# Optimization experiments

Measured on AMD Instinct MI355X. Metric: run time of the kernel, lower is better.

## Reference

```python
import jax, jax.numpy as jnp
import numpy as np

LN_EPS = 1e-5

def setup_inputs() -> dict:
    key = jax.random.key(0)
    ks = jax.random.split(key, 10)
    N, E, H, V, L, OUT, G = 100000, 600000, 128, 65, 4, 32, 64
    x_tokens = jax.random.randint(ks[0], (N, 2), 0, V, dtype=jnp.int32)
    edge_index = jax.random.randint(ks[1], (2, E), 0, N, dtype=jnp.int32)
    batch = jnp.sort(jax.random.randint(ks[2], (N,), 0, G)).astype(jnp.int64)
    s = 0.05
    key_emb = jax.random.normal(ks[3], (V, H), jnp.float32) * s
    val_emb = jax.random.normal(ks[4], (V, H), jnp.float32) * s
    Ws = jax.random.normal(ks[5], (L, H, H), jnp.float32) * (1.0 / np.sqrt(H))
    bs = jax.random.normal(ks[6], (L, H), jnp.float32) * s
    ln_g = jnp.ones((L, H), jnp.float32)
    ln_b = jnp.zeros((L, H), jnp.float32)
    out_W = jax.random.normal(ks[7], (OUT, H), jnp.float32) * (1.0 / np.sqrt(H))
    return {"x_tokens": x_tokens, "edge_index": edge_index, "batch": batch,
            "key_emb": key_emb, "val_emb": val_emb, "Ws": Ws, "bs": bs,
            "ln_g": ln_g, "ln_b": ln_b, "out_W": out_W}

def _layer_norm(x, g, b):
    mu = jnp.mean(x, axis=-1, keepdims=True)
    var = jnp.mean(jnp.square(x - mu), axis=-1, keepdims=True)
    return (x - mu) * jax.lax.rsqrt(var + LN_EPS) * g + b

def reference(x_tokens, edge_index, batch, key_emb, val_emb, Ws, bs, ln_g, ln_b, out_W):
    N = x_tokens.shape[0]
    L = Ws.shape[0]
    # layer-0: key + value embedding lookup -> [N, H]
    x = key_emb[x_tokens[:, 0]] + val_emb[x_tokens[:, 1]]
    # GCN normalization with self-loops (computed once; edges fixed per layer)
    loop = jnp.arange(N, dtype=edge_index.dtype)
    src = jnp.concatenate([edge_index[0], loop])  # [E+N]
    dst = jnp.concatenate([edge_index[1], loop])
    deg = jax.ops.segment_sum(jnp.ones_like(dst, dtype=x.dtype), dst, num_segments=N)
    dis = jnp.where(deg > 0, jax.lax.rsqrt(jnp.maximum(deg, 1.0)), 0.0)
    norm = (dis[src] * dis[dst])[:, None]  # [E+N, 1]
    for i in range(L):
        xw = x @ Ws[i]  # [N, H]
        agg = jax.ops.segment_sum(norm * xw[src], dst, num_segments=N) + bs[i]
        new_x = jax.nn.relu(agg)          # use_activation
        x = x + new_x                      # use_residual
        x = _layer_norm(x, ln_g[i], ln_b[i])  # use_layer_norm
    logits = x @ out_W.T  # Linear(bias=False) -> [N, out_dim]
    return logits
```

## Files before the change

### kernel.cpp

```cpp
#include <hip/hip_runtime.h>

#define H 128
#define LN_EPS 1e-5f

typedef unsigned short u16;
typedef unsigned int u32;
typedef __attribute__((ext_vector_type(8))) short bf16x8;
typedef __attribute__((ext_vector_type(4))) float f32x4;

__device__ __forceinline__ float bflo(u32 u){ return __uint_as_float(u << 16); }
__device__ __forceinline__ float bfhi(u32 u){ return __uint_as_float(u & 0xFFFF0000u); }
__device__ __forceinline__ float bf1(u16 u){ return __uint_as_float(((u32)u) << 16); }
__device__ __forceinline__ u16 f2bu(float f){
  u32 u = __float_as_uint(f);
  return (u16)((u + 0x7FFFu + ((u >> 16) & 1u)) >> 16);
}

__device__ __forceinline__ float ldf(const void* p, int i, bool isbf){
  return isbf ? bf1(reinterpret_cast<const u16*>(p)[i])
              : reinterpret_cast<const float*>(p)[i];
}


__global__ void k_convert(const void* __restrict__ kemb, const void* __restrict__ vemb,
                          const void* __restrict__ Ws,   const void* __restrict__ bs,
                          const void* __restrict__ lng,  const void* __restrict__ lnb,
                          const void* __restrict__ outW,
                          float* __restrict__ kemb_f, float* __restrict__ vemb_f,
                          u16* __restrict__ W_c, float* __restrict__ bs_f,
                          float* __restrict__ lng_f, float* __restrict__ lnb_f,
                          u16* __restrict__ outW_b, int* __restrict__ flag,
                          int V, int L, int OUT){
  bool isbf = (*reinterpret_cast<const u32*>(lng) == 0x3F803F80u);
  if (blockIdx.x == 0 && threadIdx.x == 0) flag[0] = isbf ? 1 : 0;
  int i = blockIdx.x * blockDim.x + threadIdx.x;
  int nEmb = V * H;
  int nW   = L * H * H;
  int nVec = L * H;
  int nOut = OUT * H;
  if (i < nEmb){ kemb_f[i] = ldf(kemb, i, isbf); vemb_f[i] = ldf(vemb, i, isbf); }
  if (i < nW){
    int j = i & 7, lane = (i >> 3) & 63, g = i >> 9;
    int s = g & 3, cg = (g >> 2) & 7, l = g >> 5;
    int k = s * 32 + (lane >> 4) * 8 + j;
    int n = cg * 16 + (lane & 15);
    W_c[i] = f2bu(ldf(Ws, l * H * H + k * H + n, isbf));
  }
  if (i < nVec){ bs_f[i] = ldf(bs, i, isbf); lng_f[i] = ldf(lng, i, isbf);
                 lnb_f[i] = ldf(lnb, i, isbf); }
  if (i < nOut){ outW_b[i] = f2bu(ldf(outW, i, isbf)); }
}


__global__ void k_count(const int* __restrict__ dst, int E, int* __restrict__ deg){
  int i = blockIdx.x * blockDim.x + threadIdx.x;
  if (i < E) atomicAdd(&deg[dst[i]], 1);
}

__device__ __forceinline__ int paddedLen(int d){ return (d + 4) & ~3; }

__global__ void k_bsum(const int* __restrict__ deg, int* __restrict__ bsum, int N){
  __shared__ int sh[256];
  int i = blockIdx.x * 256 + threadIdx.x;
  sh[threadIdx.x] = (i < N) ? paddedLen(deg[i]) : 0;
  __syncthreads();
  for (int off = 128; off > 0; off >>= 1){
    if (threadIdx.x < off) sh[threadIdx.x] += sh[threadIdx.x + off];
    __syncthreads();
  }
  if (threadIdx.x == 0) bsum[blockIdx.x] = sh[0];
}

__global__ void k_bscan(int* __restrict__ bsum, int nb){
  __shared__ int sh[1024];
  int t = threadIdx.x;
  sh[t] = (t < nb) ? bsum[t] : 0;
  __syncthreads();
  for (int off = 1; off < 1024; off <<= 1){
    int add = (t >= off) ? sh[t - off] : 0;
    __syncthreads();
    sh[t] += add;
    __syncthreads();
  }
  if (t < nb) bsum[t] = (t > 0) ? sh[t - 1] : 0;
}

__global__ void k_scan2(const int* __restrict__ deg, const int* __restrict__ bsum,
                        int* __restrict__ row_ptr, float* __restrict__ dis,
                        int* __restrict__ cursor, int2* __restrict__ csr, int N){
  __shared__ int sh[256];
  int i = blockIdx.x * 256 + threadIdx.x;
  int d = (i < N) ? deg[i] : 0;
  int v = (i < N) ? paddedLen(d) : 0;
  sh[threadIdx.x] = v;
  __syncthreads();
  for (int off = 1; off < 256; off <<= 1){
    int add = (threadIdx.x >= off) ? sh[threadIdx.x - off] : 0;
    __syncthreads();
    sh[threadIdx.x] += add;
    __syncthreads();
  }
  int excl = sh[threadIdx.x] - v + bsum[blockIdx.x];
  if (i < N){
    row_ptr[i] = excl;
    float r = rsqrtf((float)(d + 1));
    dis[i] = r;
    cursor[i] = 1;
    csr[excl] = make_int2(i * (H / 2), __float_as_int(r * r));
    for (int p = excl + d + 1; p < excl + v; p++)
      csr[p] = make_int2(0, 0);
  }
  if (i == N - 1) row_ptr[N] = excl + v;
}

__global__ void k_fill(const int* __restrict__ src, const int* __restrict__ dst, int E,
                       const float* __restrict__ dis, const int* __restrict__ row_ptr,
                       int* __restrict__ cursor, int2* __restrict__ csr){
  int i = blockIdx.x * blockDim.x + threadIdx.x;
  if (i >= E) return;
  int s = src[i], d = dst[i];
  int pos = atomicAdd(&cursor[d], 1);
  csr[row_ptr[d] + pos] = make_int2(s * (H / 2), __float_as_int(dis[s] * dis[d]));
}


__global__ __launch_bounds__(256) void k_embed(const int* __restrict__ tok,
                        const float* __restrict__ kemb, const float* __restrict__ vemb,
                        u16* __restrict__ xb, int N){
  int n = blockIdx.x * 4 + (threadIdx.x >> 6);
  if (n >= N) return;
  int h0 = (threadIdx.x & 63) * 2;
  int t0 = tok[n * 2], t1 = tok[n * 2 + 1];
  float2 k2 = *reinterpret_cast<const float2*>(&kemb[t0 * H + h0]);
  float2 v2 = *reinterpret_cast<const float2*>(&vemb[t1 * H + h0]);
  *reinterpret_cast<u32*>(&xb[(size_t)n * H + h0]) =
      (u32)f2bu(k2.x + v2.x) | ((u32)f2bu(k2.y + v2.y) << 16);
}


__global__ __launch_bounds__(256) void k_gemm(const u16* __restrict__ xb,
                                              const u16* __restrict__ Wc,
                                              u16* __restrict__ xw, int npairs){
  int wid = threadIdx.x >> 6, lane = threadIdx.x & 63;
  int sp = wid >> 1;
  int ch = wid & 1;
  int r = lane & 15, kq = lane >> 4;
  bf16x8 wf[4][4];
  #pragma unroll
  for (int c = 0; c < 4; c++)
    #pragma unroll
    for (int s = 0; s < 4; s++)
      wf[c][s] = *reinterpret_cast<const bf16x8*>(
          Wc + (size_t)((((ch * 4 + c) * 4 + s) * 64 + lane) << 3));
  for (int p = blockIdx.x; p < npairs; p += gridDim.x){
    int node0 = (p * 2 + sp) << 4;
    const u16* xrow = xb + (size_t)node0 * H + r * H + kq * 8;
    bf16x8 xf[4];
    #pragma unroll
    for (int s = 0; s < 4; s++)
      xf[s] = *reinterpret_cast<const bf16x8*>(xrow + s * 32);
    f32x4 acc[4] = {{0,0,0,0},{0,0,0,0},{0,0,0,0},{0,0,0,0}};
    #pragma unroll
    for (int s = 0; s < 4; s++)
      #pragma unroll
      for (int c = 0; c < 4; c++)
        acc[c] = __builtin_amdgcn_mfma_f32_16x16x32_bf16(wf[c][s], xf[s], acc[c], 0, 0, 0);
    u16* orow = xw + (size_t)(node0 + r) * H + ch * 64 + kq * 4;
    #pragma unroll
    for (int c = 0; c < 4; c++){
      u32 lo = (u32)f2bu(acc[c][0]) | ((u32)f2bu(acc[c][1]) << 16);
      u32 hi = (u32)f2bu(acc[c][2]) | ((u32)f2bu(acc[c][3]) << 16);
      *reinterpret_cast<uint2*>(orow + c * 16) = make_uint2(lo, hi);
    }
  }
}


__global__ __launch_bounds__(256) void k_gather(const u32* __restrict__ xw32,
    const int* __restrict__ row_ptr, const int2* __restrict__ csr,
    const float* __restrict__ bias, const float* __restrict__ gamma,
    const float* __restrict__ beta,
    u16* __restrict__ xb, int N){
  int lane = threadIdx.x & 63;
  int w = blockIdx.x * 4 + (threadIdx.x >> 6);
  int n0 = w * 2;
  if (n0 >= N) return;
  bool two = (n0 + 1 < N);
  int h0 = lane * 2;
  const int4* csr4 = reinterpret_cast<const int4*>(csr);
  int rs0 = __builtin_amdgcn_readfirstlane(row_ptr[n0]);
  int rm  = __builtin_amdgcn_readfirstlane(row_ptr[n0 + 1]);
  int re1 = two ? __builtin_amdgcn_readfirstlane(row_ptr[n0 + 2]) : rm;
  int len0 = rm - rs0, len1 = re1 - rm;
  int common = min(len0, len1);
  u32 xv0 = *reinterpret_cast<const u32*>(&xb[(size_t)n0 * H + h0]);
  u32 xv1 = two ? *reinterpret_cast<const u32*>(&xb[(size_t)(n0 + 1) * H + h0]) : 0u;
  float2 b2 = *reinterpret_cast<const float2*>(&bias[h0]);
  float2 g2 = *reinterpret_cast<const float2*>(&gamma[h0]);
  float2 t2 = *reinterpret_cast<const float2*>(&beta[h0]);
  float a00 = 0.f, a01 = 0.f, a10 = 0.f, a11 = 0.f;
#define EDGE(CX, CY, A0, A1) { \
    u32 cx = (u32)__builtin_amdgcn_readfirstlane(CX); \
    float wgt = __uint_as_float((u32)__builtin_amdgcn_readfirstlane(CY)); \
    u32 v = xw32[cx + lane]; \
    A0 = fmaf(wgt, bflo(v), A0); A1 = fmaf(wgt, bfhi(v), A1); }
  int i = 0;
  for (; i < common; i += 4){
    int4 ca = csr4[(rs0 + i) >> 1], cb = csr4[((rs0 + i) >> 1) + 1];
    int4 da = csr4[(rm + i) >> 1],  db = csr4[((rm + i) >> 1) + 1];
    EDGE(ca.x, ca.y, a00, a01) EDGE(da.x, da.y, a10, a11)
    EDGE(ca.z, ca.w, a00, a01) EDGE(da.z, da.w, a10, a11)
    EDGE(cb.x, cb.y, a00, a01) EDGE(db.x, db.y, a10, a11)
    EDGE(cb.z, cb.w, a00, a01) EDGE(db.z, db.w, a10, a11)
  }
  for (; i < len0; i += 4){
    int4 ca = csr4[(rs0 + i) >> 1], cb = csr4[((rs0 + i) >> 1) + 1];
    EDGE(ca.x, ca.y, a00, a01) EDGE(ca.z, ca.w, a00, a01)
    EDGE(cb.x, cb.y, a00, a01) EDGE(cb.z, cb.w, a00, a01)
  }
  for (; i < len1; i += 4){
    int4 da = csr4[(rm + i) >> 1], db = csr4[((rm + i) >> 1) + 1];
    EDGE(da.x, da.y, a10, a11) EDGE(da.z, da.w, a10, a11)
    EDGE(db.x, db.y, a10, a11) EDGE(db.z, db.w, a10, a11)
  }
#undef EDGE
  float v0 = fmaxf(a00 + b2.x, 0.f), v1 = fmaxf(a01 + b2.y, 0.f);
  v0 += bflo(xv0); v1 += bfhi(xv0);
  float u0 = fmaxf(a10 + b2.x, 0.f), u1 = fmaxf(a11 + b2.y, 0.f);
  u0 += bflo(xv1); u1 += bfhi(xv1);
  float s0 = v0 + v1, s1 = u0 + u1;
  #pragma unroll
  for (int off = 32; off > 0; off >>= 1){
    s0 += __shfl_xor(s0, off);
    s1 += __shfl_xor(s1, off);
  }
  float mu0 = s0 * (1.f / 128.f), mu1 = s1 * (1.f / 128.f);
  float d00 = v0 - mu0, d01 = v1 - mu0;
  float d10 = u0 - mu1, d11 = u1 - mu1;
  float q0 = d00 * d00 + d01 * d01, q1 = d10 * d10 + d11 * d11;
  #pragma unroll
  for (int off = 32; off > 0; off >>= 1){
    q0 += __shfl_xor(q0, off);
    q1 += __shfl_xor(q1, off);
  }
  float inv0 = rsqrtf(q0 * (1.f / 128.f) + LN_EPS);
  float inv1 = rsqrtf(q1 * (1.f / 128.f) + LN_EPS);
  float o00 = d00 * inv0 * g2.x + t2.x, o01 = d01 * inv0 * g2.y + t2.y;
  *reinterpret_cast<u32*>(&xb[(size_t)n0 * H + h0]) =
      (u32)f2bu(o00) | ((u32)f2bu(o01) << 16);
  if (two){
    float o10 = d10 * inv1 * g2.x + t2.x, o11 = d11 * inv1 * g2.y + t2.y;
    *reinterpret_cast<u32*>(&xb[(size_t)(n0+1) * H + h0]) =
        (u32)f2bu(o10) | ((u32)f2bu(o11) << 16);
  }
}


__global__ __launch_bounds__(256) void k_out(const u16* __restrict__ xb,
    const u16* __restrict__ oWb, u16* __restrict__ out16, float* __restrict__ outf,
    const int* __restrict__ flag, int nstrips){
  int wid = threadIdx.x >> 6, lane = threadIdx.x & 63;
  int r = lane & 15, kq = lane >> 4;
  bool isbf = (flag[0] != 0);
  bf16x8 wf[2][4];
  #pragma unroll
  for (int ct = 0; ct < 2; ct++)
    #pragma unroll
    for (int s = 0; s < 4; s++)
      wf[ct][s] = *reinterpret_cast<const bf16x8*>(
          oWb + (ct * 16 + r) * H + s * 32 + kq * 8);
  for (int strip = blockIdx.x * 4 + wid; strip < nstrips; strip += gridDim.x * 4){
    const u16* xrow = xb + (size_t)strip * 16 * H + r * H + kq * 8;
    bf16x8 xf[4];
    #pragma unroll
    for (int s = 0; s < 4; s++)
      xf[s] = *reinterpret_cast<const bf16x8*>(xrow + s * 32);
    f32x4 acc[2] = {{0,0,0,0},{0,0,0,0}};
    #pragma unroll
    for (int s = 0; s < 4; s++)
      #pragma unroll
      for (int ct = 0; ct < 2; ct++)
        acc[ct] = __builtin_amdgcn_mfma_f32_16x16x32_bf16(wf[ct][s], xf[s], acc[ct], 0, 0, 0);
    int node = strip * 16 + r;
    if (isbf){
      #pragma unroll
      for (int ct = 0; ct < 2; ct++){
        u32 lo = (u32)f2bu(acc[ct][0]) | ((u32)f2bu(acc[ct][1]) << 16);
        u32 hi = (u32)f2bu(acc[ct][2]) | ((u32)f2bu(acc[ct][3]) << 16);
        *reinterpret_cast<uint2*>(out16 + (size_t)node * 32 + ct * 16 + kq * 4) =
            make_uint2(lo, hi);
      }
    } else {
      #pragma unroll
      for (int ct = 0; ct < 2; ct++)
        *reinterpret_cast<f32x4*>(outf + (size_t)node * 32 + ct * 16 + kq * 4) = acc[ct];
    }
  }
}


extern "C" void kernel_launch(void* const* d_in, const int* in_sizes, int n_in,
                              void* d_out, int out_size, void* d_ws, size_t ws_size,
                              hipStream_t stream){
  const int*  x_tokens = (const int*)d_in[0];
  const int*  edge_idx = (const int*)d_in[1];
  const void* kemb = d_in[3];
  const void* vemb = d_in[4];
  const void* Ws   = d_in[5];
  const void* bs   = d_in[6];
  const void* lng  = d_in[7];
  const void* lnb  = d_in[8];
  const void* outW = d_in[9];

  int N   = in_sizes[0] / 2;
  int E   = in_sizes[1] / 2;
  int V   = in_sizes[3] / H;
  int L   = in_sizes[5] / (H * H);
  int OUT = in_sizes[9] / H;

  char* ws = (char*)d_ws;
  size_t off = 0;
  auto alloc = [&](size_t bytes) -> void* {
    void* p = ws + off;
    off += (bytes + 255) & ~(size_t)255;
    return p;
  };
  u16*   xb     = (u16*)  alloc((size_t)N * H * 2);
  u16*   xw     = (u16*)  alloc((size_t)N * H * 2);
  int*   deg    = (int*)  alloc((size_t)N * 4);
  int*   cursor = (int*)  alloc((size_t)N * 4);
  int*   row_ptr= (int*)  alloc((size_t)(N + 1) * 4);
  float* dis    = (float*)alloc((size_t)N * 4);
  int*   bsum   = (int*)  alloc(1024 * 4);
  int2*  csr    = (int2*) alloc(((size_t)E + 4 * (size_t)N) * 8);
  float* kemb_f = (float*)alloc((size_t)V * H * 4);
  float* vemb_f = (float*)alloc((size_t)V * H * 4);
  u16*   W_c    = (u16*)  alloc((size_t)L * H * H * 2);
  float* bs_f   = (float*)alloc((size_t)L * H * 4);
  float* lng_f  = (float*)alloc((size_t)L * H * 4);
  float* lnb_f  = (float*)alloc((size_t)L * H * 4);
  u16*   outW_b = (u16*)  alloc((size_t)OUT * H * 2);
  int*   flag   = (int*)  alloc(256);

  const int* esrc = edge_idx;
  const int* edst = edge_idx + E;

  (void)hipMemsetAsync(deg, 0, (size_t)N * 4, stream);

  int convTotal = L * H * H;
  int cb = (convTotal + 255) / 256;
  k_convert<<<cb, 256, 0, stream>>>(kemb, vemb, Ws, bs, lng, lnb, outW,
                                    kemb_f, vemb_f, W_c, bs_f, lng_f, lnb_f,
                                    outW_b, flag, V, L, OUT);

  int eb = (E + 255) / 256;
  int nb = (N + 255) / 256;
  k_count<<<eb, 256, 0, stream>>>(edst, E, deg);
  k_bsum <<<nb, 256, 0, stream>>>(deg, bsum, N);
  k_bscan<<<1, 1024, 0, stream>>>(bsum, nb);
  k_scan2<<<nb, 256, 0, stream>>>(deg, bsum, row_ptr, dis, cursor, csr, N);
  k_fill <<<eb, 256, 0, stream>>>(esrc, edst, E, dis, row_ptr, cursor, csr);
  k_embed<<<(N + 3) / 4, 256, 0, stream>>>(x_tokens, kemb_f, vemb_f, xb, N);

  int nstrips = N / 16;
  int npairs  = nstrips / 2;
  int gwaves  = (N + 1) / 2;
  for (int l = 0; l < L; l++){
    k_gemm  <<<1024, 256, 0, stream>>>(xb, W_c + (size_t)l * H * H, xw, npairs);
    k_gather<<<(gwaves + 3) / 4, 256, 0, stream>>>((const u32*)xw, row_ptr, csr,
                                                   bs_f + l * H, lng_f + l * H,
                                                   lnb_f + l * H, xb, N);
  }
  k_out<<<(nstrips + 3) / 4, 256, 0, stream>>>(xb, outW_b, (u16*)d_out, (float*)d_out,
                                               flag, nstrips);
}
```

Measured before the change: 318.0 us.

## Fuse gather+layernorm with next layer's GEMM and output projection via LDS tile

```diff
diff --git a/kernel.cpp b/kernel.cpp
--- a/kernel.cpp
+++ b/kernel.cpp
@@ -2,6 +2,7 @@
 
 #define H 128
 #define LN_EPS 1e-5f
+#define TROW 66
 
 typedef unsigned short u16;
 typedef unsigned int u32;
@@ -176,17 +177,21 @@
 }
 
 
-__global__ __launch_bounds__(256) void k_gather(const u32* __restrict__ xw32,
+__device__ __forceinline__ void gather2(const u32* __restrict__ xw32,
     const int* __restrict__ row_ptr, const int2* __restrict__ csr,
     const float* __restrict__ bias, const float* __restrict__ gamma,
     const float* __restrict__ beta,
-    u16* __restrict__ xb, int N){
+    u16* __restrict__ xb, int N, u32* __restrict__ tile, bool writeGlobal){
   int lane = threadIdx.x & 63;
-  int w = blockIdx.x * 4 + (threadIdx.x >> 6);
-  int n0 = w * 2;
-  if (n0 >= N) return;
+  int w = threadIdx.x >> 6;
+  int n0 = blockIdx.x * 16 + 2 * w;
+  int h0 = lane * 2;
+  if (n0 >= N){
+    tile[(2 * w) * TROW + lane] = 0;
+    tile[(2 * w + 1) * TROW + lane] = 0;
+    return;
+  }
   bool two = (n0 + 1 < N);
-  int h0 = lane * 2;
   const int4* csr4 = reinterpret_cast<const int4*>(csr);
   int rs0 = __builtin_amdgcn_readfirstlane(row_ptr[n0]);
   int rm  = __builtin_amdgcn_readfirstlane(row_ptr[n0 + 1]);
@@ -245,56 +250,84 @@
   }
   float inv0 = rsqrtf(q0 * (1.f / 128.f) + LN_EPS);
   float inv1 = rsqrtf(q1 * (1.f / 128.f) + LN_EPS);
-  float o00 = d00 * inv0 * g2.x + t2.x, o01 = d01 * inv0 * g2.y + t2.y;
-  *reinterpret_cast<u32*>(&xb[(size_t)n0 * H + h0]) =
-      (u32)f2bu(o00) | ((u32)f2bu(o01) << 16);
-  if (two){
-    float o10 = d10 * inv1 * g2.x + t2.x, o11 = d11 * inv1 * g2.y + t2.y;
-    *reinterpret_cast<u32*>(&xb[(size_t)(n0+1) * H + h0]) =
-        (u32)f2bu(o10) | ((u32)f2bu(o11) << 16);
-  }
-}
-
-
-__global__ __launch_bounds__(256) void k_out(const u16* __restrict__ xb,
-    const u16* __restrict__ oWb, u16* __restrict__ out16, float* __restrict__ outf,
-    const int* __restrict__ flag, int nstrips){
-  int wid = threadIdx.x >> 6, lane = threadIdx.x & 63;
+  u32 w0 = (u32)f2bu(d00 * inv0 * g2.x + t2.x) |
+           ((u32)f2bu(d01 * inv0 * g2.y + t2.y) << 16);
+  u32 w1 = (u32)f2bu(d10 * inv1 * g2.x + t2.x) |
+           ((u32)f2bu(d11 * inv1 * g2.y + t2.y) << 16);
+  tile[(2 * w) * TROW + lane] = w0;
+  tile[(2 * w + 1) * TROW + lane] = two ? w1 : 0u;
+  if (writeGlobal){
+    *reinterpret_cast<u32*>(&xb[(size_t)n0 * H + h0]) = w0;
+    if (two)
+      *reinterpret_cast<u32*>(&xb[(size_t)(n0 + 1) * H + h0]) = w1;
+  }
+}
+
+__global__ __launch_bounds__(512) void k_fgemm(const u32* __restrict__ xw32,
+    const int* __restrict__ row_ptr, const int2* __restrict__ csr,
+    const float* __restrict__ bias, const float* __restrict__ gamma,
+    const float* __restrict__ beta,
+    u16* __restrict__ xb, const u16* __restrict__ Wc,
+    u16* __restrict__ xw_out, int N){
+  __shared__ u32 tile[16 * TROW];
+  int lane = threadIdx.x & 63, w = threadIdx.x >> 6;
   int r = lane & 15, kq = lane >> 4;
-  bool isbf = (flag[0] != 0);
-  bf16x8 wf[2][4];
-  #pragma unroll
-  for (int ct = 0; ct < 2; ct++)
+  bf16x8 wfr[4];
+  #pragma unroll
+  for (int s = 0; s < 4; s++)
+    wfr[s] = *reinterpret_cast<const bf16x8*>(Wc + (size_t)(((w * 4 + s) * 64 + lane) << 3));
+  gather2(xw32, row_ptr, csr, bias, gamma, beta, xb, N, tile, true);
+  __syncthreads();
+  int node = blockIdx.x * 16 + r;
+  if (node >= N) return;
+  const u16* t16 = reinterpret_cast<const u16*>(tile);
+  f32x4 acc = {0.f, 0.f, 0.f, 0.f};
+  #pragma unroll
+  for (int s = 0; s < 4; s++){
+    bf16x8 xf = *reinterpret_cast<const bf16x8*>(t16 + r * (2 * TROW) + s * 32 + kq * 8);
+    acc = __builtin_amdgcn_mfma_f32_16x16x32_bf16(wfr[s], xf, acc, 0, 0, 0);
+  }
+  u32 lo = (u32)f2bu(acc[0]) | ((u32)f2bu(acc[1]) << 16);
+  u32 hi = (u32)f2bu(acc[2]) | ((u32)f2bu(acc[3]) << 16);
+  *reinterpret_cast<uint2*>(xw_out + (size_t)node * H + w * 16 + kq * 4) =
+      make_uint2(lo, hi);
+}
+
+__global__ __launch_bounds__(512) void k_fout(const u32* __restrict__ xw32,
+    const int* __restrict__ row_ptr, const int2* __restrict__ csr,
+    const float* __restrict__ bias, const float* __restrict__ gamma,
+    const float* __restrict__ beta,
+    u16* __restrict__ xb, const u16* __restrict__ oWb,
+    u16* __restrict__ out16, float* __restrict__ outf,
+    const int* __restrict__ flag, int N){
+  __shared__ u32 tile[16 * TROW];
+  int lane = threadIdx.x & 63, w = threadIdx.x >> 6;
+  int r = lane & 15, kq = lane >> 4;
+  bf16x8 wfr[4];
+  if (w < 2){
     #pragma unroll
     for (int s = 0; s < 4; s++)
-      wf[ct][s] = *reinterpret_cast<const bf16x8*>(
-          oWb + (ct * 16 + r) * H + s * 32 + kq * 8);
-  for (int strip = blockIdx.x * 4 + wid; strip < nstrips; strip += gridDim.x * 4){
-    const u16* xrow = xb + (size_t)strip * 16 * H + r * H + kq * 8;
-    bf16x8 xf[4];
-    #pragma unroll
-    for (int s = 0; s < 4; s++)
-      xf[s] = *reinterpret_cast<const bf16x8*>(xrow + s * 32);
-    f32x4 acc[2] = {{0,0,0,0},{0,0,0,0}};
-    #pragma unroll
-    for (int s = 0; s < 4; s++)
-      #pragma unroll
-      for (int ct = 0; ct < 2; ct++)
-        acc[ct] = __builtin_amdgcn_mfma_f32_16x16x32_bf16(wf[ct][s], xf[s], acc[ct], 0, 0, 0);
-    int node = strip * 16 + r;
-    if (isbf){
-      #pragma unroll
-      for (int ct = 0; ct < 2; ct++){
-        u32 lo = (u32)f2bu(acc[ct][0]) | ((u32)f2bu(acc[ct][1]) << 16);
-        u32 hi = (u32)f2bu(acc[ct][2]) | ((u32)f2bu(acc[ct][3]) << 16);
-        *reinterpret_cast<uint2*>(out16 + (size_t)node * 32 + ct * 16 + kq * 4) =
-            make_uint2(lo, hi);
-      }
-    } else {
-      #pragma unroll
-      for (int ct = 0; ct < 2; ct++)
-        *reinterpret_cast<f32x4*>(outf + (size_t)node * 32 + ct * 16 + kq * 4) = acc[ct];
-    }
+      wfr[s] = *reinterpret_cast<const bf16x8*>(oWb + (w * 16 + r) * H + s * 32 + kq * 8);
+  }
+  gather2(xw32, row_ptr, csr, bias, gamma, beta, xb, N, tile, false);
+  __syncthreads();
+  if (w >= 2) return;
+  int node = blockIdx.x * 16 + r;
+  if (node >= N) return;
+  const u16* t16 = reinterpret_cast<const u16*>(tile);
+  f32x4 acc = {0.f, 0.f, 0.f, 0.f};
+  #pragma unroll
+  for (int s = 0; s < 4; s++){
+    bf16x8 xf = *reinterpret_cast<const bf16x8*>(t16 + r * (2 * TROW) + s * 32 + kq * 8);
+    acc = __builtin_amdgcn_mfma_f32_16x16x32_bf16(wfr[s], xf, acc, 0, 0, 0);
+  }
+  if (flag[0]){
+    u32 lo = (u32)f2bu(acc[0]) | ((u32)f2bu(acc[1]) << 16);
+    u32 hi = (u32)f2bu(acc[2]) | ((u32)f2bu(acc[3]) << 16);
+    *reinterpret_cast<uint2*>(out16 + (size_t)node * 32 + w * 16 + kq * 4) =
+        make_uint2(lo, hi);
+  } else {
+    *reinterpret_cast<f32x4*>(outf + (size_t)node * 32 + w * 16 + kq * 4) = acc;
   }
 }
 
@@ -326,7 +359,8 @@
     return p;
   };
   u16*   xb     = (u16*)  alloc((size_t)N * H * 2);
-  u16*   xw     = (u16*)  alloc((size_t)N * H * 2);
+  u16*   xwA    = (u16*)  alloc((size_t)N * H * 2);
+  u16*   xwB    = (u16*)  alloc((size_t)N * H * 2);
   int*   deg    = (int*)  alloc((size_t)N * 4);
   int*   cursor = (int*)  alloc((size_t)N * 4);
   int*   row_ptr= (int*)  alloc((size_t)(N + 1) * 4);
@@ -362,15 +396,20 @@
   k_fill <<<eb, 256, 0, stream>>>(esrc, edst, E, dis, row_ptr, cursor, csr);
   k_embed<<<(N + 3) / 4, 256, 0, stream>>>(x_tokens, kemb_f, vemb_f, xb, N);
 
-  int nstrips = N / 16;
-  int npairs  = nstrips / 2;
-  int gwaves  = (N + 1) / 2;
-  for (int l = 0; l < L; l++){
-    k_gemm  <<<1024, 256, 0, stream>>>(xb, W_c + (size_t)l * H * H, xw, npairs);
-    k_gather<<<(gwaves + 3) / 4, 256, 0, stream>>>((const u32*)xw, row_ptr, csr,
-                                                   bs_f + l * H, lng_f + l * H,
-                                                   lnb_f + l * H, xb, N);
-  }
-  k_out<<<(nstrips + 3) / 4, 256, 0, stream>>>(xb, outW_b, (u16*)d_out, (float*)d_out,
-                                               flag, nstrips);
-}
+  int nstrips = (N + 15) / 16;
+  int npairs  = (nstrips + 1) / 2;
+  k_gemm<<<1024, 256, 0, stream>>>(xb, W_c, xwA, npairs);
+  u16* xw_in = xwA; u16* xw_out = xwB;
+  for (int l = 0; l < L - 1; l++){
+    k_fgemm<<<nstrips, 512, 0, stream>>>((const u32*)xw_in, row_ptr, csr,
+                                         bs_f + l * H, lng_f + l * H, lnb_f + l * H,
+                                         xb, W_c + (size_t)(l + 1) * H * H,
+                                         xw_out, N);
+    u16* t = xw_in; xw_in = xw_out; xw_out = t;
+  }
+  k_fout<<<nstrips, 512, 0, stream>>>((const u32*)xw_in, row_ptr, csr,
+                                      bs_f + (L - 1) * H, lng_f + (L - 1) * H,
+                                      lnb_f + (L - 1) * H,
+                                      xb, outW_b, (u16*)d_out, (float*)d_out,
+                                      flag, N);
+}
```

New measurement: 297.2 us. 1.07x faster.
